# Kernel tuning notes

Hardware: AMD Instinct MI355X
Metric: run time of the kernel (lower is better)

The kernel has to match this reference:

```python
import jax, jax.numpy as jnp
import numpy as np

N_NODES = 100000


def _gcn_conv(x, W, b, src, dst, n):
    # PyG GCNConv: add self-loops, sym-normalize by deg^{-1/2}, then X W + b
    h = x @ W  # [N, out]
    ones = jnp.ones(src.shape[0], dtype=x.dtype)
    deg = jax.ops.segment_sum(ones, dst, num_segments=n) + 1.0  # +1 for self loop
    dinv = jax.lax.rsqrt(deg)
    norm = dinv[src] * dinv[dst]  # [E]
    agg = jax.ops.segment_sum(h[src] * norm[:, None], dst, num_segments=n)
    agg = agg + h * (dinv * dinv)[:, None]  # self-loop contribution
    return agg + b


def setup_inputs() -> dict:
    key = jax.random.key(0)
    k1, k2, k3, k4 = jax.random.split(key, 4)
    n, e = N_NODES, 1600000
    in_d, hid_d, out_d = 128, 128, 64
    x = jax.random.normal(k1, (n, in_d), dtype=jnp.float32)
    edge_index = jax.random.randint(k2, (2, e), 0, n, dtype=jnp.int64)
    s1 = 1.0 / np.sqrt(in_d)
    s2 = 1.0 / np.sqrt(hid_d)
    W1 = jax.random.uniform(k3, (in_d, hid_d), jnp.float32, -s1, s1)
    W2 = jax.random.uniform(k4, (hid_d, out_d), jnp.float32, -s2, s2)
    b1 = jnp.zeros((hid_d,), jnp.float32)
    b2 = jnp.zeros((out_d,), jnp.float32)
    return {"x": x, "edge_index": edge_index, "W1": W1, "b1": b1, "W2": W2, "b2": b2}


def reference(x, edge_index, W1, b1, W2, b2):
    src, dst = edge_index[0], edge_index[1]
    n = x.shape[0]
    h = _gcn_conv(x, W1, b1, src, dst, n)
    h = jax.nn.relu(h)
    # dropout p=0.2 is identity at eval time
    out = _gcn_conv(h, W2, b2, src, dst, n)
    return out
```

## Files before the change

### kernel.cpp

```cpp
#include <hip/hip_runtime.h>


typedef unsigned int u32;
using bfrag = __attribute__((ext_vector_type(8))) short;
using f4    = __attribute__((ext_vector_type(4))) float;

__device__ inline u32 pack_bf16(float a, float b) {
    u32 ua = __float_as_uint(a);
    u32 ub = __float_as_uint(b);
    ua += 0x7fffu + ((ua >> 16) & 1u);
    ub += 0x7fffu + ((ub >> 16) & 1u);
    return (ua >> 16) | (ub & 0xffff0000u);
}
__device__ inline float bf_lo(u32 v) { return __uint_as_float(v << 16); }
__device__ inline float bf_hi(u32 v) { return __uint_as_float(v & 0xffff0000u); }

__device__ inline u32 pack_w(float w) {
    u32 b = __float_as_uint(w) + 0x800u;
    if (b < 0x3B800000u) b = 0x3B800000u;
    if (b > 0x3F800000u) b = 0x3F800000u;
    return (b - 0x3B800000u) >> 12;
}
__device__ inline float dec_w(u32 e) {
    return __uint_as_float(((e & 0x7fffu) << 12) + 0x3B800000u);
}

__device__ inline bfrag as_bfrag(uint4 v) {
    union { uint4 u; bfrag b; } x; x.u = v; return x.b;
}

__device__ inline void prep_w_chunk(int idx, const float* __restrict__ W1,
                                    const float* __restrict__ W2,
                                    u32* __restrict__ W1t, u32* __restrict__ W2t) {
    if (idx < 128 * 64) {
        int nr = idx >> 6, kd = idx & 63;
        W1t[idx] = pack_bf16(W1[(2 * kd) * 128 + nr], W1[(2 * kd + 1) * 128 + nr]);
    } else if (idx < 128 * 64 + 64 * 64) {
        int i = idx - 128 * 64;
        int nr = i >> 6, kd = i & 63;
        W2t[i] = pack_bf16(W2[(2 * kd) * 64 + nr], W2[(2 * kd + 1) * 64 + nr]);
    }
}


__global__ __launch_bounds__(256) void count_bins_pw(const int* __restrict__ dst,
                                                     int* __restrict__ bc,
                                                     int E, int nbin, int nb3, int M,
                                                     const float* __restrict__ W1,
                                                     const float* __restrict__ W2,
                                                     u32* __restrict__ W1t,
                                                     u32* __restrict__ W2t) {
    __shared__ int hist[512];
    if (blockIdx.x >= (unsigned)nb3) {
        prep_w_chunk((blockIdx.x - nb3) * 256 + threadIdx.x, W1, W2, W1t, W2t);
        return;
    }
    if (blockIdx.x == 0 && threadIdx.x == 0) bc[M] = E;
    for (int t = threadIdx.x; t < nbin; t += 256) hist[t] = 0;
    __syncthreads();
    const int base = blockIdx.x * 2048 + threadIdx.x;
#pragma unroll
    for (int k = 0; k < 8; ++k) {
        int e = base + k * 256;
        if (e < E) atomicAdd(&hist[dst[e] >> 8], 1);
    }
    __syncthreads();
    for (int t = threadIdx.x; t < nbin; t += 256)
        bc[(size_t)t * nb3 + blockIdx.x] = hist[t];
}

__global__ __launch_bounds__(1024) void scan_reduce_g(const int* __restrict__ a,
                                                      int* __restrict__ bsum, int M) {
    __shared__ int wsum[16];
    int i = blockIdx.x * 1024 + threadIdx.x;
    int v = (i < M) ? a[i] : 0;
#pragma unroll
    for (int off = 32; off > 0; off >>= 1) v += __shfl_down(v, off);
    const int lane = threadIdx.x & 63;
    const int wid  = threadIdx.x >> 6;
    if (lane == 0) wsum[wid] = v;
    __syncthreads();
    if (threadIdx.x < 16) {
        int s = wsum[threadIdx.x];
#pragma unroll
        for (int off = 8; off > 0; off >>= 1) s += __shfl_down(s, off);
        if (threadIdx.x == 0) bsum[blockIdx.x] = s;
    }
}

__global__ __launch_bounds__(1024) void scan_apply_g2(int* __restrict__ a,
                                                      const int* __restrict__ bsum,
                                                      int nb, int M) {
    __shared__ int wsum[16];
    __shared__ int base_s;
    const int lane = threadIdx.x & 63;
    const int wid  = threadIdx.x >> 6;
    int pv = 0;
    for (int t = threadIdx.x; t < (int)blockIdx.x; t += 1024) pv += bsum[t];
#pragma unroll
    for (int off = 32; off > 0; off >>= 1) pv += __shfl_down(pv, off);
    if (lane == 0) wsum[wid] = pv;
    __syncthreads();
    if (threadIdx.x == 0) {
        int s = 0;
#pragma unroll
        for (int w = 0; w < 16; ++w) s += wsum[w];
        base_s = s;
    }
    __syncthreads();
    const int boff = base_s;
    int i = blockIdx.x * 1024 + threadIdx.x;
    int v = (i < M) ? a[i] : 0;
    int x = v;
#pragma unroll
    for (int off = 1; off < 64; off <<= 1) {
        int t = __shfl_up(x, off);
        if (lane >= off) x += t;
    }
    if (lane == 63) wsum[wid] = x;
    __syncthreads();
    if (wid == 0 && lane < 16) {
        int w = wsum[lane];
#pragma unroll
        for (int off = 1; off < 16; off <<= 1) {
            int t = __shfl_up(w, off);
            if (lane >= off) w += t;
        }
        wsum[lane] = w;
    }
    __syncthreads();
    int wave_excl = (wid == 0) ? 0 : wsum[wid - 1];
    if (i < M) a[i] = boff + wave_excl + (x - v);
}

__global__ __launch_bounds__(256) void scatter_bins(const int* __restrict__ src,
                                                    const int* __restrict__ dst,
                                                    const int* __restrict__ offs,
                                                    u32* __restrict__ tmp,
                                                    int E, int nbin, int nb3) {
    __shared__ int cur[512];
    for (int t = threadIdx.x; t < nbin; t += 256)
        cur[t] = offs[(size_t)t * nb3 + blockIdx.x];
    __syncthreads();
    const int base = blockIdx.x * 2048 + threadIdx.x;
#pragma unroll
    for (int k = 0; k < 8; ++k) {
        int e = base + k * 256;
        if (e < E) {
            int d = dst[e];
            int pos = atomicAdd(&cur[d >> 8], 1);
            tmp[pos] = ((u32)(d & 255) << 17) | (u32)src[e];
        }
    }
}

__global__ __launch_bounds__(256) void bucket_csr2(const u32* __restrict__ tmp,
                                                   const int* __restrict__ offs,
                                                   u32* __restrict__ tmp3,
                                                   int* __restrict__ row_ptr,
                                                   float* __restrict__ dinv,
                                                   int n, int nb3, int E) {
    __shared__ int hist[256];
    __shared__ int cur[256];
    __shared__ int wtot[4];
    const int b   = blockIdx.x;
    const int beg = offs[(size_t)b * nb3];
    const int end = offs[(size_t)(b + 1) * nb3];
    hist[threadIdx.x] = 0;
    __syncthreads();
    for (int i = beg + threadIdx.x; i < end; i += 256)
        atomicAdd(&hist[tmp[i] >> 17], 1);
    __syncthreads();
    const int lane = threadIdx.x & 63;
    const int wid  = threadIdx.x >> 6;
    int v = hist[threadIdx.x];
    int x = v;
#pragma unroll
    for (int off = 1; off < 64; off <<= 1) {
        int t = __shfl_up(x, off);
        if (lane >= off) x += t;
    }
    if (lane == 63) wtot[wid] = x;
    __syncthreads();
    int wbase = 0;
    for (int w = 0; w < wid; ++w) wbase += wtot[w];
    const int rp = beg + wbase + x - v;
    cur[threadIdx.x] = rp;
    const int d = b * 256 + threadIdx.x;
    if (d < n) {
        row_ptr[d] = rp;
        dinv[d]    = rsqrtf((float)v + 1.0f);
    }
    if (b == 0 && threadIdx.x == 0) row_ptr[n] = E;
    __syncthreads();
    for (int i = beg + threadIdx.x; i < end; i += 256) {
        u32 r = tmp[i];
        int pos = atomicAdd(&cur[r >> 17], 1);
        tmp3[pos] = r & 0x1ffffu;
    }
}

__global__ __launch_bounds__(256) void build_ew2(const u32* __restrict__ tmp3,
                                                 const int* __restrict__ row_ptr,
                                                 const float* __restrict__ dinv,
                                                 u32* __restrict__ ew, int n) {
    __shared__ int   sh_rp[257];
    __shared__ float sh_di[256];
    const int b = blockIdx.x;
    const int t = threadIdx.x;
    const int base = b * 256;
    const int idx  = base + t;
    sh_rp[t] = row_ptr[(idx <= n) ? idx : n];
    if (t == 0) {
        int last = base + 256;
        sh_rp[256] = row_ptr[(last <= n) ? last : n];
    }
    sh_di[t] = (idx < n) ? dinv[idx] : 0.0f;
    __syncthreads();
    const int beg = sh_rp[0];
    const int end = sh_rp[256];
    for (int i = beg + t; i < end; i += 256) {
        u32 s = tmp3[i];
        int lo = 0, hi = 255;
#pragma unroll
        for (int st = 0; st < 8; ++st) {
            int mid = (lo + hi + 1) >> 1;
            if (sh_rp[mid] <= i) lo = mid; else hi = mid - 1;
        }
        ew[i] = (s << 15) | pack_w(dinv[s] * sh_di[lo]);
    }
}


template <int OUT, bool ABF>
__global__ __launch_bounds__(256) void gemm_mfma(const void* __restrict__ Ap,
                                                 const u32* __restrict__ Wt,
                                                 u32* __restrict__ C, int n) {
    constexpr int NT = OUT / 16;
    const int lane = threadIdx.x & 63;
    const int wv   = threadIdx.x >> 6;
    const int r15  = lane & 15;
    const int quad = lane >> 4;
    const int rowbase = blockIdx.x * 128 + wv * 32;

    bfrag af[2][4];
#pragma unroll
    for (int mi = 0; mi < 2; ++mi) {
        int row = rowbase + mi * 16 + r15;
        row = (row < n) ? row : (n - 1);
        if constexpr (ABF) {
            const u32* ar = (const u32*)Ap + (size_t)row * 64 + quad * 4;
#pragma unroll
            for (int ks = 0; ks < 4; ++ks)
                af[mi][ks] = as_bfrag(*(const uint4*)(ar + ks * 16));
        } else {
            const float* arf = (const float*)Ap + (size_t)row * 128 + quad * 8;
#pragma unroll
            for (int ks = 0; ks < 4; ++ks) {
                float4 v0 = *(const float4*)(arf + ks * 32);
                float4 v1 = *(const float4*)(arf + ks * 32 + 4);
                uint4 p;
                p.x = pack_bf16(v0.x, v0.y);
                p.y = pack_bf16(v0.z, v0.w);
                p.z = pack_bf16(v1.x, v1.y);
                p.w = pack_bf16(v1.z, v1.w);
                af[mi][ks] = as_bfrag(p);
            }
        }
    }

    f4 acc[2][NT];
#pragma unroll
    for (int mi = 0; mi < 2; ++mi)
#pragma unroll
        for (int nt = 0; nt < NT; ++nt) acc[mi][nt] = (f4)0.0f;

#pragma unroll
    for (int nt = 0; nt < NT; ++nt) {
        const u32* wr = Wt + (size_t)(nt * 16 + r15) * 64 + quad * 4;
#pragma unroll
        for (int ks = 0; ks < 4; ++ks) {
            bfrag bf = as_bfrag(*(const uint4*)(wr + ks * 16));
            acc[0][nt] = __builtin_amdgcn_mfma_f32_16x16x32_bf16(bf, af[0][ks], acc[0][nt], 0, 0, 0);
            acc[1][nt] = __builtin_amdgcn_mfma_f32_16x16x32_bf16(bf, af[1][ks], acc[1][nt], 0, 0, 0);
        }
    }

#pragma unroll
    for (int mi = 0; mi < 2; ++mi) {
        int row = rowbase + mi * 16 + r15;
        if (row < n) {
            u32* cp = C + (size_t)row * (OUT / 2);
#pragma unroll
            for (int nt = 0; nt < NT; ++nt) {
                uint2 p;
                p.x = pack_bf16(acc[mi][nt][0], acc[mi][nt][1]);
                p.y = pack_bf16(acc[mi][nt][2], acc[mi][nt][3]);
                *(uint2*)(cp + nt * 8 + quad * 2) = p;
            }
        }
    }
}


__global__ __launch_bounds__(256) void gather128(const u32* __restrict__ h,
                                                 const float* __restrict__ dinv,
                                                 const int* __restrict__ row_ptr,
                                                 const u32* __restrict__ ew,
                                                 const float* __restrict__ bias,
                                                 u32* __restrict__ outp, int n) {
    const int lane = threadIdx.x & 63;
    int node = blockIdx.x * 4 + (threadIdx.x >> 6);
    if (node >= n) return;
    node = __builtin_amdgcn_readfirstlane(node);

    const float dd  = dinv[node];
    const int   beg = __builtin_amdgcn_readfirstlane(row_ptr[node]);
    const int   end = __builtin_amdgcn_readfirstlane(row_ptr[node + 1]);

    u32 sv = h[(size_t)node * 64 + lane];
    float2 b = ((const float2*)bias)[lane];
    float acc0 = fmaf(bf_lo(sv) * dd, dd, b.x);
    float acc1 = fmaf(bf_hi(sv) * dd, dd, b.y);

    int j = beg;
    for (; j + 16 <= end; j += 16) {
        u32 ep[16];
#pragma unroll
        for (int k = 0; k < 16; ++k) ep[k] = ew[j + k];
        u32 v[16];
#pragma unroll
        for (int k = 0; k < 16; ++k)
            v[k] = h[((size_t)(ep[k] >> 15) << 6) + lane];
#pragma unroll
        for (int k = 0; k < 16; ++k) {
            float wf = dec_w(ep[k]);
            acc0 = fmaf(wf, bf_lo(v[k]), acc0);
            acc1 = fmaf(wf, bf_hi(v[k]), acc1);
        }
    }
    for (; j < end; j += 8) {
        const int cnt = end - j;
        u32 ep[8];
#pragma unroll
        for (int k = 0; k < 8; ++k) {
            int c = j + k;
            ep[k] = ew[(c < end) ? c : end - 1];
        }
        u32 v[8];
#pragma unroll
        for (int k = 0; k < 8; ++k)
            v[k] = h[((size_t)(ep[k] >> 15) << 6) + lane];
#pragma unroll
        for (int k = 0; k < 8; ++k) {
            float wf = (k < cnt) ? dec_w(ep[k]) : 0.0f;
            acc0 = fmaf(wf, bf_lo(v[k]), acc0);
            acc1 = fmaf(wf, bf_hi(v[k]), acc1);
        }
    }

    outp[(size_t)node * 64 + lane] = pack_bf16(fmaxf(acc0, 0.0f), fmaxf(acc1, 0.0f));
}

__global__ __launch_bounds__(256) void gather64(const u32* __restrict__ h,
                                                const float* __restrict__ dinv,
                                                const int* __restrict__ row_ptr,
                                                const u32* __restrict__ ew,
                                                const float* __restrict__ bias,
                                                float* __restrict__ outp, int n) {
    const int lane   = threadIdx.x & 63;
    const int lane32 = lane & 31;
    const int sub    = lane >> 5;
    int node = blockIdx.x * 4 + (threadIdx.x >> 6);
    if (node >= n) return;
    node = __builtin_amdgcn_readfirstlane(node);

    const int beg = __builtin_amdgcn_readfirstlane(row_ptr[node]);
    const int end = __builtin_amdgcn_readfirstlane(row_ptr[node + 1]);

    float acc0 = 0.0f, acc1 = 0.0f;
    if (sub == 0) {
        const float dd = dinv[node];
        u32 sv = h[(size_t)node * 32 + lane32];
        float2 b = ((const float2*)bias)[lane32];
        acc0 = fmaf(bf_lo(sv) * dd, dd, b.x);
        acc1 = fmaf(bf_hi(sv) * dd, dd, b.y);
    }

    int j = beg;
    for (; j + 16 <= end; j += 16) {
        u32 ep[16];
#pragma unroll
        for (int k = 0; k < 16; ++k) ep[k] = ew[j + k];
        u32 v[8]; float wl[8];
#pragma unroll
        for (int p = 0; p < 8; ++p) {
            u32 e0 = ep[2 * p], e1 = ep[2 * p + 1];
            u32 so = sub ? (e1 >> 15) : (e0 >> 15);
            wl[p]  = sub ? dec_w(e1) : dec_w(e0);
            v[p]   = h[((size_t)so << 5) + lane32];
        }
#pragma unroll
        for (int p = 0; p < 8; ++p) {
            acc0 = fmaf(wl[p], bf_lo(v[p]), acc0);
            acc1 = fmaf(wl[p], bf_hi(v[p]), acc1);
        }
    }
    for (; j < end; j += 8) {
        const int cnt = end - j;
        u32 ep[8];
#pragma unroll
        for (int k = 0; k < 8; ++k) {
            int c = j + k;
            ep[k] = ew[(c < end) ? c : end - 1];
        }
        u32 v[4]; float wl[4];
#pragma unroll
        for (int p = 0; p < 4; ++p) {
            u32 e0 = ep[2 * p], e1 = ep[2 * p + 1];
            float w0 = (2 * p     < cnt) ? dec_w(e0) : 0.0f;
            float w1 = (2 * p + 1 < cnt) ? dec_w(e1) : 0.0f;
            u32 so = sub ? (e1 >> 15) : (e0 >> 15);
            wl[p]  = sub ? w1 : w0;
            v[p]   = h[((size_t)so << 5) + lane32];
        }
#pragma unroll
        for (int p = 0; p < 4; ++p) {
            acc0 = fmaf(wl[p], bf_lo(v[p]), acc0);
            acc1 = fmaf(wl[p], bf_hi(v[p]), acc1);
        }
    }

    acc0 += __shfl_xor(acc0, 32);
    acc1 += __shfl_xor(acc1, 32);
    if (sub == 0)
        ((float2*)(outp + (size_t)node * 64))[lane32] = make_float2(acc0, acc1);
}

extern "C" void kernel_launch(void* const* d_in, const int* in_sizes, int n_in,
                              void* d_out, int out_size, void* d_ws, size_t ws_size,
                              hipStream_t stream) {
    const float* x  = (const float*)d_in[0];
    const int*   ei = (const int*)d_in[1];
    const float* W1 = (const float*)d_in[2];
    const float* b1 = (const float*)d_in[3];
    const float* W2 = (const float*)d_in[4];
    const float* b2 = (const float*)d_in[5];
    float*       out = (float*)d_out;

    const int n = in_sizes[0] / 128;
    const int E = in_sizes[1] / 2;
    const int* srcv = ei;
    const int* dstv = ei + E;

    const int NP = 102400;
    u32* wsd = (u32*)d_ws;
    float* dinv    = (float*)wsd;
    int*   row_ptr = (int*)(wsd + NP);
    u32*   ew      = wsd + 2 * (size_t)NP;
    u32*   h1u     = ew + E;
    u32*   agg1b   = h1u + (size_t)n * 64;
    u32*   W1t     = agg1b + (size_t)n * 64;
    u32*   W2t     = W1t + 8192;
    u32*   h2u     = h1u;

    int*   bco  = (int*)(h1u + 131072);
    u32*   tmp2 = h1u + 524288;
    u32*   tmp3 = tmp2 + (size_t)E;
    int*   bsum = (int*)(h1u + 4000000);

    const int NBIN = (n + 255) >> 8;
    const int NB3  = (E + 2047) / 2048;
    const int M    = NBIN * NB3;
    const int MB   = (M + 1023) / 1024;

    count_bins_pw<<<NB3 + 48, 256, 0, stream>>>(dstv, bco, E, NBIN, NB3, M,
                                                W1, W2, W1t, W2t);
    scan_reduce_g<<<MB, 1024, 0, stream>>>(bco, bsum, M);
    scan_apply_g2<<<MB, 1024, 0, stream>>>(bco, bsum, MB, M);
    scatter_bins<<<NB3, 256, 0, stream>>>(srcv, dstv, bco, tmp2, E, NBIN, NB3);
    bucket_csr2<<<NBIN, 256, 0, stream>>>(tmp2, bco, tmp3, row_ptr, dinv, n, NB3, E);
    build_ew2<<<NBIN, 256, 0, stream>>>(tmp3, row_ptr, dinv, ew, n);

    const int gblocks = (n + 127) / 128;
    gemm_mfma<128, false><<<gblocks, 256, 0, stream>>>(x, W1t, h1u, n);
    gather128<<<(n + 3) / 4, 256, 0, stream>>>(h1u, dinv, row_ptr, ew, b1, agg1b, n);

    gemm_mfma<64, true><<<gblocks, 256, 0, stream>>>(agg1b, W2t, h2u, n);
    gather64<<<(n + 3) / 4, 256, 0, stream>>>(h2u, dinv, row_ptr, ew, b2, out, n);
}
```

Measured before the change: 294.1 us.

## Fuse bucket scatter with edge-weight build and co-launch first GEMM

Removes the tmp3 intermediate by having the second bucket pass compute packed edge weights directly at the scatter position, replacing the binary search over row_ptr. The first-layer GEMM is merged into the same launch as extra blocks, so the dense matmul runs alongside the irregular CSR work and one launch is saved. Scratch buffers move into the agg1b region so that h1u can be written concurrently. In exchange, the histogram pass now re-reads tmp and edge ordering within a row stays atomic-dependent.

```diff
diff --git a/kernel.cpp b/kernel.cpp
--- a/kernel.cpp
+++ b/kernel.cpp
@@ -39,6 +39,77 @@
         int i = idx - 128 * 64;
         int nr = i >> 6, kd = i & 63;
         W2t[i] = pack_bf16(W2[(2 * kd) * 64 + nr], W2[(2 * kd + 1) * 64 + nr]);
+    }
+}
+
+
+template <int OUT, bool ABF>
+__device__ inline void gemm_body(int bid, const void* __restrict__ Ap,
+                                 const u32* __restrict__ Wt,
+                                 u32* __restrict__ C, int n) {
+    constexpr int NT = OUT / 16;
+    const int lane = threadIdx.x & 63;
+    const int wv   = threadIdx.x >> 6;
+    const int r15  = lane & 15;
+    const int quad = lane >> 4;
+    const int rowbase = bid * 128 + wv * 32;
+
+    bfrag af[2][4];
+#pragma unroll
+    for (int mi = 0; mi < 2; ++mi) {
+        int row = rowbase + mi * 16 + r15;
+        row = (row < n) ? row : (n - 1);
+        if constexpr (ABF) {
+            const u32* ar = (const u32*)Ap + (size_t)row * 64 + quad * 4;
+#pragma unroll
+            for (int ks = 0; ks < 4; ++ks)
+                af[mi][ks] = as_bfrag(*(const uint4*)(ar + ks * 16));
+        } else {
+            const float* arf = (const float*)Ap + (size_t)row * 128 + quad * 8;
+#pragma unroll
+            for (int ks = 0; ks < 4; ++ks) {
+                float4 v0 = *(const float4*)(arf + ks * 32);
+                float4 v1 = *(const float4*)(arf + ks * 32 + 4);
+                uint4 p;
+                p.x = pack_bf16(v0.x, v0.y);
+                p.y = pack_bf16(v0.z, v0.w);
+                p.z = pack_bf16(v1.x, v1.y);
+                p.w = pack_bf16(v1.z, v1.w);
+                af[mi][ks] = as_bfrag(p);
+            }
+        }
+    }
+
+    f4 acc[2][NT];
+#pragma unroll
+    for (int mi = 0; mi < 2; ++mi)
+#pragma unroll
+        for (int nt = 0; nt < NT; ++nt) acc[mi][nt] = (f4)0.0f;
+
+#pragma unroll
+    for (int nt = 0; nt < NT; ++nt) {
+        const u32* wr = Wt + (size_t)(nt * 16 + r15) * 64 + quad * 4;
+#pragma unroll
+        for (int ks = 0; ks < 4; ++ks) {
+            bfrag bf = as_bfrag(*(const uint4*)(wr + ks * 16));
+            acc[0][nt] = __builtin_amdgcn_mfma_f32_16x16x32_bf16(bf, af[0][ks], acc[0][nt], 0, 0, 0);
+            acc[1][nt] = __builtin_amdgcn_mfma_f32_16x16x32_bf16(bf, af[1][ks], acc[1][nt], 0, 0, 0);
+        }
+    }
+
+#pragma unroll
+    for (int mi = 0; mi < 2; ++mi) {
+        int row = rowbase + mi * 16 + r15;
+        if (row < n) {
+            u32* cp = C + (size_t)row * (OUT / 2);
+#pragma unroll
+            for (int nt = 0; nt < NT; ++nt) {
+                uint2 p;
+                p.x = pack_bf16(acc[mi][nt][0], acc[mi][nt][1]);
+                p.y = pack_bf16(acc[mi][nt][2], acc[mi][nt][3]);
+                *(uint2*)(cp + nt * 8 + quad * 2) = p;
+            }
+        }
     }
 }
 
@@ -154,14 +225,12 @@
     }
 }
 
-__global__ __launch_bounds__(256) void bucket_csr2(const u32* __restrict__ tmp,
+__global__ __launch_bounds__(256) void bucket_hist(const u32* __restrict__ tmp,
                                                    const int* __restrict__ offs,
-                                                   u32* __restrict__ tmp3,
                                                    int* __restrict__ row_ptr,
                                                    float* __restrict__ dinv,
                                                    int n, int nb3, int E) {
     __shared__ int hist[256];
-    __shared__ int cur[256];
     __shared__ int wtot[4];
     const int b   = blockIdx.x;
     const int beg = offs[(size_t)b * nb3];
@@ -185,49 +254,40 @@
     int wbase = 0;
     for (int w = 0; w < wid; ++w) wbase += wtot[w];
     const int rp = beg + wbase + x - v;
-    cur[threadIdx.x] = rp;
     const int d = b * 256 + threadIdx.x;
     if (d < n) {
         row_ptr[d] = rp;
         dinv[d]    = rsqrtf((float)v + 1.0f);
     }
     if (b == 0 && threadIdx.x == 0) row_ptr[n] = E;
-    __syncthreads();
-    for (int i = beg + threadIdx.x; i < end; i += 256) {
-        u32 r = tmp[i];
-        int pos = atomicAdd(&cur[r >> 17], 1);
-        tmp3[pos] = r & 0x1ffffu;
-    }
-}
-
-__global__ __launch_bounds__(256) void build_ew2(const u32* __restrict__ tmp3,
-                                                 const int* __restrict__ row_ptr,
-                                                 const float* __restrict__ dinv,
-                                                 u32* __restrict__ ew, int n) {
-    __shared__ int   sh_rp[257];
-    __shared__ float sh_di[256];
+}
+
+__global__ __launch_bounds__(256) void bucket_ew_gemm1(
+    const u32* __restrict__ tmp, const int* __restrict__ offs,
+    const int* __restrict__ row_ptr, const float* __restrict__ dinv,
+    u32* __restrict__ ew, int n, int nb3, int nbin,
+    const float* __restrict__ x, const u32* __restrict__ W1t,
+    u32* __restrict__ h1u) {
+    if (blockIdx.x >= (unsigned)nbin) {
+        gemm_body<128, false>(blockIdx.x - nbin, x, W1t, h1u, n);
+        return;
+    }
+    __shared__ int   cur[256];
+    __shared__ float sdi[256];
     const int b = blockIdx.x;
     const int t = threadIdx.x;
-    const int base = b * 256;
-    const int idx  = base + t;
-    sh_rp[t] = row_ptr[(idx <= n) ? idx : n];
-    if (t == 0) {
-        int last = base + 256;
-        sh_rp[256] = row_ptr[(last <= n) ? last : n];
-    }
-    sh_di[t] = (idx < n) ? dinv[idx] : 0.0f;
-    __syncthreads();
-    const int beg = sh_rp[0];
-    const int end = sh_rp[256];
+    const int beg = offs[(size_t)b * nb3];
+    const int end = offs[(size_t)(b + 1) * nb3];
+    const int d = b * 256 + t;
+    cur[t] = row_ptr[(d <= n) ? d : n];
+    sdi[t] = (d < n) ? dinv[d] : 0.0f;
+    __syncthreads();
     for (int i = beg + t; i < end; i += 256) {
-        u32 s = tmp3[i];
-        int lo = 0, hi = 255;
-#pragma unroll
-        for (int st = 0; st < 8; ++st) {
-            int mid = (lo + hi + 1) >> 1;
-            if (sh_rp[mid] <= i) lo = mid; else hi = mid - 1;
-        }
-        ew[i] = (s << 15) | pack_w(dinv[s] * sh_di[lo]);
+        u32 r = tmp[i];
+        int k = r >> 17;
+        int pos = atomicAdd(&cur[k], 1);
+        u32 s = r & 0x1ffffu;
+        ew[pos] = (s << 15) | pack_w(dinv[s] * sdi[k]);
     }
 }
 
@@ -236,70 +296,7 @@
 __global__ __launch_bounds__(256) void gemm_mfma(const void* __restrict__ Ap,
                                                  const u32* __restrict__ Wt,
                                                  u32* __restrict__ C, int n) {
-    constexpr int NT = OUT / 16;
-    const int lane = threadIdx.x & 63;
-    const int wv   = threadIdx.x >> 6;
-    const int r15  = lane & 15;
-    const int quad = lane >> 4;
-    const int rowbase = blockIdx.x * 128 + wv * 32;
-
-    bfrag af[2][4];
-#pragma unroll
-    for (int mi = 0; mi < 2; ++mi) {
-        int row = rowbase + mi * 16 + r15;
-        row = (row < n) ? row : (n - 1);
-        if constexpr (ABF) {
-            const u32* ar = (const u32*)Ap + (size_t)row * 64 + quad * 4;
-#pragma unroll
-            for (int ks = 0; ks < 4; ++ks)
-                af[mi][ks] = as_bfrag(*(const uint4*)(ar + ks * 16));
-        } else {
-            const float* arf = (const float*)Ap + (size_t)row * 128 + quad * 8;
-#pragma unroll
-            for (int ks = 0; ks < 4; ++ks) {
-                float4 v0 = *(const float4*)(arf + ks * 32);
-                float4 v1 = *(const float4*)(arf + ks * 32 + 4);
-                uint4 p;
-                p.x = pack_bf16(v0.x, v0.y);
-                p.y = pack_bf16(v0.z, v0.w);
-                p.z = pack_bf16(v1.x, v1.y);
-                p.w = pack_bf16(v1.z, v1.w);
-                af[mi][ks] = as_bfrag(p);
-            }
-        }
-    }
-
-    f4 acc[2][NT];
-#pragma unroll
-    for (int mi = 0; mi < 2; ++mi)
-#pragma unroll
-        for (int nt = 0; nt < NT; ++nt) acc[mi][nt] = (f4)0.0f;
-
-#pragma unroll
-    for (int nt = 0; nt < NT; ++nt) {
-        const u32* wr = Wt + (size_t)(nt * 16 + r15) * 64 + quad * 4;
-#pragma unroll
-        for (int ks = 0; ks < 4; ++ks) {
-            bfrag bf = as_bfrag(*(const uint4*)(wr + ks * 16));
-            acc[0][nt] = __builtin_amdgcn_mfma_f32_16x16x32_bf16(bf, af[0][ks], acc[0][nt], 0, 0, 0);
-            acc[1][nt] = __builtin_amdgcn_mfma_f32_16x16x32_bf16(bf, af[1][ks], acc[1][nt], 0, 0, 0);
-        }
-    }
-
-#pragma unroll
-    for (int mi = 0; mi < 2; ++mi) {
-        int row = rowbase + mi * 16 + r15;
-        if (row < n) {
-            u32* cp = C + (size_t)row * (OUT / 2);
-#pragma unroll
-            for (int nt = 0; nt < NT; ++nt) {
-                uint2 p;
-                p.x = pack_bf16(acc[mi][nt][0], acc[mi][nt][1]);
-                p.y = pack_bf16(acc[mi][nt][2], acc[mi][nt][3]);
-                *(uint2*)(cp + nt * 8 + quad * 2) = p;
-            }
-        }
-    }
+    gemm_body<OUT, ABF>(blockIdx.x, Ap, Wt, C, n);
 }
 
 
@@ -464,26 +461,27 @@
     u32*   W2t     = W1t + 8192;
     u32*   h2u     = h1u;
 
-    int*   bco  = (int*)(h1u + 131072);
-    u32*   tmp2 = h1u + 524288;
-    u32*   tmp3 = tmp2 + (size_t)E;
-    int*   bsum = (int*)(h1u + 4000000);
+    int*   bco  = (int*)agg1b;
+    u32*   tmp2 = agg1b + 400000;
+    int*   bsum = (int*)(agg1b + 2200000);
 
     const int NBIN = (n + 255) >> 8;
     const int NB3  = (E + 2047) / 2048;
     const int M    = NBIN * NB3;
     const int MB   = (M + 1023) / 1024;
+
+    const int gblocks = (n + 127) / 128;
 
     count_bins_pw<<<NB3 + 48, 256, 0, stream>>>(dstv, bco, E, NBIN, NB3, M,
                                                 W1, W2, W1t, W2t);
     scan_reduce_g<<<MB, 1024, 0, stream>>>(bco, bsum, M);
     scan_apply_g2<<<MB, 1024, 0, stream>>>(bco, bsum, MB, M);
     scatter_bins<<<NB3, 256, 0, stream>>>(srcv, dstv, bco, tmp2, E, NBIN, NB3);
-    bucket_csr2<<<NBIN, 256, 0, stream>>>(tmp2, bco, tmp3, row_ptr, dinv, n, NB3, E);
-    build_ew2<<<NBIN, 256, 0, stream>>>(tmp3, row_ptr, dinv, ew, n);
-
-    const int gblocks = (n + 127) / 128;
-    gemm_mfma<128, false><<<gblocks, 256, 0, stream>>>(x, W1t, h1u, n);
+    bucket_hist<<<NBIN, 256, 0, stream>>>(tmp2, bco, row_ptr, dinv, n, NB3, E);
+    bucket_ew_gemm1<<<NBIN + gblocks, 256, 0, stream>>>(tmp2, bco, row_ptr, dinv,
+                                                        ew, n, NB3, NBIN,
+                                                        x, W1t, h1u);
+
     gather128<<<(n + 3) / 4, 256, 0, stream>>>(h1u, dinv, row_ptr, ew, b1, agg1b, n);
 
     gemm_mfma<64, true><<<gblocks, 256, 0, stream>>>(agg1b, W2t, h2u, n);
```

Result: no change. 290.1 us (-1.3%).
